# Kernel optimization log

Hardware: AMD Instinct MI355X
Metric: run time of the kernel (lower is better)

Reference implementation:

```python
import jax, jax.numpy as jnp
import numpy as np
import math

NEG = -1e9
NUM_SQUEEZE = 2


def seq_mask(lengths, max_len, dtype):
    return (jnp.arange(max_len)[None, :] < lengths[:, None]).astype(dtype)


def maximum_path(logp, attn_mask, x_lengths, y_lengths):
    """Monotonic alignment search (Viterbi DP). logp, attn_mask: [B, Tx, Ty]."""
    B, Tx, Ty = logp.shape
    logp = jnp.where(attn_mask > 0, logp, NEG)
    cols = jnp.moveaxis(logp, 2, 0)  # [Ty, B, Tx]

    v0 = jnp.where(jnp.arange(Tx)[None, :] == 0, 0.0, NEG).astype(logp.dtype)
    v0 = jnp.broadcast_to(v0, (B, Tx))

    def fwd(v, col):
        v_shift = jnp.concatenate([jnp.full((B, 1), NEG, logp.dtype), v[:, :-1]], axis=1)
        v_new = col + jnp.maximum(v, v_shift)
        return v_new, v_new

    _, values = jax.lax.scan(fwd, v0, cols)  # [Ty, B, Tx] DP table

    def bwd(index, j):
        active = j < y_lengths  # [B]
        row = jax.nn.one_hot(index, Tx, dtype=logp.dtype) * active[:, None].astype(logp.dtype)
        vprev = values[jnp.maximum(j - 1, 0)]  # [B, Tx]
        v_here = jnp.take_along_axis(vprev, index[:, None], axis=1)[:, 0]
        v_left = jnp.take_along_axis(vprev, jnp.maximum(index - 1, 0)[:, None], axis=1)[:, 0]
        dec = (index != 0) & ((index == j) | (v_here < v_left)) & active & (j > 0)
        return jnp.where(dec, index - 1, index), row

    js = jnp.arange(Ty - 1, -1, -1)
    _, rows = jax.lax.scan(bwd, x_lengths - 1, js)  # reversed j order
    path = jnp.moveaxis(jnp.flip(rows, 0), 0, 2)  # [B, Tx, Ty]
    return path * attn_mask


def setup_inputs() -> dict:
    key = jax.random.key(0)
    ks = jax.random.split(key, 6)
    B, C, Ten, Tde = 32, 80, 512, 2048
    return {
        "o_mean": jax.random.normal(ks[0], (B, C, Ten), jnp.float32),
        "o_log_scale": jax.random.normal(ks[1], (B, C, Ten), jnp.float32) * 0.1,
        "o_dur_log": jax.random.normal(ks[2], (B, 1, Ten), jnp.float32),
        "z": jax.random.normal(ks[3], (B, C, Tde), jnp.float32),
        "x_lengths": jax.random.randint(ks[4], (B,), Ten // 2, Ten + 1, jnp.int32),
        "y_lengths": jax.random.randint(ks[5], (B,), Tde // 2, Tde + 1, jnp.int32),
    }


def reference(o_mean, o_log_scale, o_dur_log, z, x_lengths, y_lengths):
    B, C, Ten = o_mean.shape
    Tde = z.shape[2]
    dt = o_mean.dtype

    # preprocess: floor y_lengths to multiple of num_squeeze
    y_lengths = (y_lengths // NUM_SQUEEZE) * NUM_SQUEEZE

    x_mask = seq_mask(x_lengths, Ten, dt)[:, None, :]   # [B,1,Tx]
    y_mask = seq_mask(y_lengths, Tde, dt)[:, None, :]   # [B,1,Ty]
    attn_mask = x_mask[:, 0, :, None] * y_mask[:, 0, None, :]  # [B,Tx,Ty]

    z = z * y_mask  # decoder output is masked

    # log-likelihood terms (torch.no_grad in original)
    o_scale = jnp.exp(-2.0 * o_log_scale)                       # [B,C,Tx]
    logp1 = jnp.sum(-0.5 * math.log(2 * math.pi) - o_log_scale, axis=1)[:, :, None]
    logp2 = jnp.einsum('bct,bcs->bts', o_scale, -0.5 * z * z)   # [B,Tx,Ty]
    logp3 = jnp.einsum('bct,bcs->bts', o_mean * o_scale, z)
    logp4 = jnp.sum(-0.5 * o_mean * o_mean * o_scale, axis=1)[:, :, None]
    logp = logp1 + logp2 + logp3 + logp4

    attn = maximum_path(logp, attn_mask, x_lengths, y_lengths)  # [B,Tx,Ty] hard path

    # compute_outputs
    y_mean = jnp.einsum('bts,bct->bcs', attn, o_mean)           # [B,C,Ty]
    y_log_scale = jnp.einsum('bts,bct->bcs', attn, o_log_scale)
    o_attn_dur = jnp.log1p(jnp.sum(attn, axis=-1))[:, None, :] * x_mask  # [B,1,Tx]

    return (
        jnp.transpose(z, (0, 2, 1)),            # z: [B,Ty,C]
        jnp.transpose(y_mean, (0, 2, 1)),       # y_mean: [B,Ty,C]
        jnp.transpose(y_log_scale, (0, 2, 1)),  # y_log_scale: [B,Ty,C]
        jnp.transpose(attn, (0, 2, 1)),         # alignments: [B,Ty,Tx]
        jnp.transpose(o_dur_log, (0, 2, 1)),    # durations_log: [B,Tx,1]
        jnp.transpose(o_attn_dur, (0, 2, 1)),   # total_durations_log: [B,Tx,1]
    )
```

## Files before the change

kernel.cpp:

```cpp
#include <hip/hip_runtime.h>
#include <math.h>

#define BB  32
#define CC  80
#define TXX 512
#define TYY 2048
#define NEGV -1e9f

typedef float v2f __attribute__((ext_vector_type(2)));

__global__ __launch_bounds__(256) void k_prep(
    const float* __restrict__ om, const float* __restrict__ ols,
    float* __restrict__ SA, float* __restrict__ SB,
    float* __restrict__ L1, float* __restrict__ L4,
    float* __restrict__ OMTf, float* __restrict__ OLSTf,
    int* __restrict__ DUR)
{
    int b = blockIdx.y;
    int t0 = blockIdx.x * 64;
    int tid = threadIdx.x;
    int cl = tid >> 6;
    int tl = tid & 63;
    __shared__ float sm[64][81], sl[64][81], ssa[64][81];
    #pragma unroll
    for (int cp = 0; cp < 20; ++cp) {
        int c = cp * 4 + cl;
        size_t gidx = ((size_t)b * CC + c) * TXX + t0 + tl;
        float m = om[gidx], ls = ols[gidx];
        float sa = expf(-2.0f * ls);
        SA[gidx] = sa;
        SB[gidx] = m * sa;
        sm[tl][c] = m; sl[tl][c] = ls; ssa[tl][c] = sa;
    }
    __syncthreads();
    if (tid < 64) {
        float l1 = 0.f, l4 = 0.f;
        #pragma unroll 4
        for (int c = 0; c < CC; ++c) {
            float m = sm[tid][c], ls = sl[tid][c], sa = ssa[tid][c];
            l1 += (-0.9189385332046727f - ls);
            l4 += ((-0.5f * m) * m) * sa;
        }
        int g = b * TXX + t0 + tid;
        L1[g] = l1; L4[g] = l4; DUR[g] = 0;
    }
    size_t obase = (size_t)b * TXX * CC + (size_t)t0 * CC;
    for (int e = tid; e < 64 * CC; e += 256) {
        int t = e / CC, c = e - t * CC;
        OMTf[obase + e]  = sm[t][c];
        OLSTf[obase + e] = sl[t][c];
    }
}

__global__ __launch_bounds__(256) void k_logp(
    const float* __restrict__ SA, const float* __restrict__ SB,
    const float* __restrict__ L1, const float* __restrict__ L4,
    const float* __restrict__ z,
    const int* __restrict__ xlp, const int* __restrict__ ylp,
    float* __restrict__ logp)
{
    int b = blockIdx.z;
    int ylen = (ylp[b] >> 1) << 1;
    int s0 = blockIdx.y * 128;
    if (s0 >= ylen) return;
    int t0 = blockIdx.x * 64;
    int xlen = xlp[b];
    int tid = threadIdx.x;

    __shared__ float sA[16][64], sB[16][64], sZ[16][128], sW[16][128];

    v2f acc2[4][4], acc3[4][4];
    #pragma unroll
    for (int i = 0; i < 4; ++i)
        #pragma unroll
        for (int p = 0; p < 4; ++p) { acc2[i][p] = (v2f){0.f, 0.f}; acc3[i][p] = (v2f){0.f, 0.f}; }

    int tt = (tid & 15) << 2;
    int ss = (tid >> 4) << 3;
    int r  = tid >> 4;
    int c4 = (tid & 15) << 2;
    int s8 = (tid & 15) << 3;

    for (int c0 = 0; c0 < CC; c0 += 16) {
        const float* pa = SA + ((size_t)b * CC + (c0 + r)) * TXX + t0 + c4;
        const float* pb = SB + ((size_t)b * CC + (c0 + r)) * TXX + t0 + c4;
        float4 va = *(const float4*)pa;
        float4 vb = *(const float4*)pb;
        *(float4*)&sA[r][c4] = va;
        *(float4*)&sB[r][c4] = vb;

        const float* pz = z + ((size_t)b * CC + (c0 + r)) * TYY + s0 + s8;
        float4 q0 = *(const float4*)pz;
        float4 q1 = *(const float4*)(pz + 4);
        float zf[8] = {q0.x, q0.y, q0.z, q0.w, q1.x, q1.y, q1.z, q1.w};
        #pragma unroll
        for (int i = 0; i < 8; ++i) {
            sZ[r][s8 + i] = zf[i];
            sW[r][s8 + i] = (-0.5f * zf[i]) * zf[i];
        }
        __syncthreads();
        #pragma unroll
        for (int kc = 0; kc < 16; ++kc) {
            float4 a2 = *(const float4*)&sA[kc][tt];
            float4 a3 = *(const float4*)&sB[kc][tt];
            const v2f* zp = (const v2f*)&sZ[kc][ss];
            const v2f* wp = (const v2f*)&sW[kc][ss];
            v2f bz[4] = {zp[0], zp[1], zp[2], zp[3]};
            v2f bw[4] = {wp[0], wp[1], wp[2], wp[3]};
            float av2[4] = {a2.x, a2.y, a2.z, a2.w};
            float av3[4] = {a3.x, a3.y, a3.z, a3.w};
            #pragma unroll
            for (int i = 0; i < 4; ++i) {
                v2f d2 = {av2[i], av2[i]};
                v2f d3 = {av3[i], av3[i]};
                #pragma unroll
                for (int p = 0; p < 4; ++p) {
                    acc2[i][p] = __builtin_elementwise_fma(d2, bw[p], acc2[i][p]);
                    acc3[i][p] = __builtin_elementwise_fma(d3, bz[p], acc3[i][p]);
                }
            }
        }
        __syncthreads();
    }

    float l1a[4], l4a[4]; int bad[4];
    #pragma unroll
    for (int i = 0; i < 4; ++i) {
        int t = t0 + tt + i;
        l1a[i] = L1[b * TXX + t];
        l4a[i] = L4[b * TXX + t];
        bad[i] = (t >= xlen);
    }
    #pragma unroll
    for (int p = 0; p < 4; ++p) {
        #pragma unroll
        for (int h = 0; h < 2; ++h) {
            int s = s0 + ss + 2 * p + h;
            float vals[4];
            #pragma unroll
            for (int i = 0; i < 4; ++i) {
                float a2v = h ? acc2[i][p].y : acc2[i][p].x;
                float a3v = h ? acc3[i][p].y : acc3[i][p].x;
                float v = ((l1a[i] + a2v) + a3v) + l4a[i];
                vals[i] = bad[i] ? NEGV : v;
            }
            float4 o; o.x = vals[0]; o.y = vals[1]; o.z = vals[2]; o.w = vals[3];
            *(float4*)&logp[((size_t)b * TYY + s) * TXX + t0 + tt] = o;
        }
    }
}

__device__ __forceinline__ unsigned dp_bits(const float v[8], float left) {
    unsigned by = (v[0] < left) ? 1u : 0u;
    by |= (v[1] < v[0]) ? 2u   : 0u;
    by |= (v[2] < v[1]) ? 4u   : 0u;
    by |= (v[3] < v[2]) ? 8u   : 0u;
    by |= (v[4] < v[3]) ? 16u  : 0u;
    by |= (v[5] < v[4]) ? 32u  : 0u;
    by |= (v[6] < v[5]) ? 64u  : 0u;
    by |= (v[7] < v[6]) ? 128u : 0u;
    return by;
}
__device__ __forceinline__ void dp_core(float v[8], float4 c0, float4 c1, float left) {
    float m0 = fmaxf(v[0], left);
    float m1 = fmaxf(v[1], v[0]);
    float m2 = fmaxf(v[2], v[1]);
    float m3 = fmaxf(v[3], v[2]);
    float m4 = fmaxf(v[4], v[3]);
    float m5 = fmaxf(v[5], v[4]);
    float m6 = fmaxf(v[6], v[5]);
    float m7 = fmaxf(v[7], v[6]);
    v[0] = c0.x + m0; v[1] = c0.y + m1; v[2] = c0.z + m2; v[3] = c0.w + m3;
    v[4] = c1.x + m4; v[5] = c1.y + m5; v[6] = c1.z + m6; v[7] = c1.w + m7;
}

__global__ __launch_bounds__(64) void k_fwd(
    const float* __restrict__ logp, const int* __restrict__ ylp,
    unsigned char* __restrict__ BITS)
{
    int b = blockIdx.x, lane = threadIdx.x;
    int n = (ylp[b] >> 1) << 1;
    int nm1 = n - 1;
    const float* lp = logp + (size_t)b * TYY * TXX + lane * 8;
    unsigned char* BITSb = BITS + (size_t)b * TYY * 64;
    __shared__ unsigned char lbits[128 * 64];

    float v[8];
    #pragma unroll
    for (int k = 0; k < 8; ++k) v[k] = NEGV;
    if (lane == 0) v[0] = 0.0f;

    float4 p0[16], p1[16];
    #pragma unroll
    for (int i = 0; i < 16; ++i) {
        int r0 = (i < nm1) ? i : nm1;
        p0[i] = *(const float4*)(lp + (size_t)r0 * TXX);
        p1[i] = *(const float4*)(lp + (size_t)r0 * TXX + 4);
    }

    int gs = 0;
    for (; gs + 64 <= n; gs += 64) {
        int hb = gs & 127;
        unsigned char* lb_first = lbits + lane + (((hb + 127) & 127) << 6);
        unsigned char* lb_rest  = lbits + lane + (hb << 6);
        #pragma unroll
        for (int j4 = 0; j4 < 4; ++j4) {
            #pragma unroll
            for (int uu = 0; uu < 16; ++uu) {
                const int j = j4 * 16 + uu;
                float4 c0 = p0[uu], c1 = p1[uu];
                int pr = gs + j + 16; if (pr > nm1) pr = nm1;
                p0[uu] = *(const float4*)(lp + (size_t)pr * TXX);
                p1[uu] = *(const float4*)(lp + (size_t)pr * TXX + 4);
                float left = __shfl_up(v[7], 1, 64);
                if (lane == 0) left = NEGV;
                if (j > 0 || gs > 0) {
                    unsigned by = dp_bits(v, left);
                    if (j == 0) *lb_first = (unsigned char)by;
                    else        lb_rest[(j - 1) << 6] = (unsigned char)by;
                }
                dp_core(v, c0, c1, left);
            }
        }
        if (gs >= 64) {
            int ps = hb ^ 64;
            const uint4* srcl = (const uint4*)(lbits + (size_t)((ps + lane) << 6));
            uint4 q0 = srcl[0], q1 = srcl[1], q2 = srcl[2], q3 = srcl[3];
            uint4* dstl = (uint4*)(BITSb + ((size_t)(gs - 64 + lane) << 6));
            dstl[0] = q0; dstl[1] = q1; dstl[2] = q2; dstl[3] = q3;
        }
    }
    {
        int pbase = gs - 64;
        int ps = pbase & 127;
        if (lane < 63) {
            const uint4* srcl = (const uint4*)(lbits + (size_t)((ps + lane) << 6));
            uint4 q0 = srcl[0], q1 = srcl[1], q2 = srcl[2], q3 = srcl[3];
            uint4* dstl = (uint4*)(BITSb + ((size_t)(pbase + lane) << 6));
            dstl[0] = q0; dstl[1] = q1; dstl[2] = q2; dstl[3] = q3;
        }
    }
    unsigned char* brow = BITSb + lane;
    #pragma unroll
    for (int j = 0; j < 64; ++j) {
        int scur = gs + j;
        if (scur >= n) break;
        const int uu = j & 15;
        float4 c0 = p0[uu], c1 = p1[uu];
        int pr = scur + 16; if (pr > nm1) pr = nm1;
        p0[uu] = *(const float4*)(lp + (size_t)pr * TXX);
        p1[uu] = *(const float4*)(lp + (size_t)pr * TXX + 4);
        float left = __shfl_up(v[7], 1, 64);
        if (lane == 0) left = NEGV;
        unsigned by = dp_bits(v, left);
        brow[(size_t)(scur - 1) << 6] = (unsigned char)by;
        dp_core(v, c0, c1, left);
    }
}

__global__ __launch_bounds__(64) void k_bwd(
    const unsigned char* __restrict__ BITS, const int* __restrict__ xlp,
    const int* __restrict__ ylp, int* __restrict__ TSTAR, int* __restrict__ DUR)
{
    int b = blockIdx.x, lane = threadIdx.x;
    int ylen = (ylp[b] >> 1) << 1;
    int xlen = xlp[b];
    const unsigned char* bb = BITS + (size_t)b * TYY * 64;
    int* tst = TSTAR + b * TYY;
    int idx = xlen - 1;
    int j0 = ylen - 1;
    while (j0 >= 0) {
        int steps = (j0 + 1 < 32) ? (j0 + 1) : 32;
        int row = j0 - 1 - lane;
        int bw = idx >> 5; if (bw > 0) --bw;
        int base_bit = bw << 5;
        unsigned w0 = 0u, w1 = 0u;
        if (lane < steps && row >= 0) {
            const unsigned* rp = (const unsigned*)(bb + (size_t)row * 64);
            w0 = rp[bw]; w1 = rp[bw + 1];
        }
        unsigned long long wq = (((unsigned long long)w1) << 32) | w0;
        int saved = 0;
        #pragma unroll
        for (int k = 0; k < 32; ++k) {
            if (k >= steps) break;
            int j = j0 - k;
            if (lane == k) saved = idx;
            unsigned long long wk = __shfl(wq, k, 64);
            unsigned bit = (unsigned)(wk >> (idx - base_bit)) & 1u;
            int dec = (idx != 0 && j > 0 && (idx == j || bit)) ? 1 : 0;
            idx -= dec;
        }
        if (lane < steps) {
            tst[j0 - lane] = saved;
            atomicAdd(&DUR[b * TXX + saved], 1);
        }
        j0 -= steps;
    }
}

__global__ __launch_bounds__(256) void k_small(
    const float* __restrict__ odur, const int* __restrict__ xlp,
    const int* __restrict__ DUR, float* __restrict__ out4,
    float* __restrict__ out5)
{
    int gid = blockIdx.x * 256 + threadIdx.x;
    int b = gid >> 9, t = gid & 511;
    out4[gid] = odur[gid];
    int xlen = xlp[b];
    float d = (float)DUR[gid];
    out5[gid] = (t < xlen) ? log1pf(d) : 0.0f;
}

__global__ __launch_bounds__(256) void k_out_sc(
    const float* __restrict__ z, const float* __restrict__ OMTf,
    const float* __restrict__ OLSTf, const int* __restrict__ TSTAR,
    const int* __restrict__ ylp,
    float* __restrict__ out0, float* __restrict__ out1,
    float* __restrict__ out2)
{
    int b = blockIdx.y;
    int s0 = blockIdx.x * 32;
    int tid = threadIdx.x;
    int ylen = (ylp[b] >> 1) << 1;
    __shared__ int sT[32];
    __shared__ float zt[32][81];
    if (tid < 32) {
        int s = s0 + tid;
        sT[tid] = (s < ylen) ? TSTAR[b * TYY + s] : 0;
    }
    int c_l = tid >> 5, s_l = tid & 31;
    #pragma unroll
    for (int cp = 0; cp < 10; ++cp) {
        int c = cp * 8 + c_l;
        zt[s_l][c] = z[((size_t)b * CC + c) * TYY + s0 + s_l];
    }
    __syncthreads();
    for (int e = tid; e < 32 * 80; e += 256) {
        int sl = e / 80;
        int cc = e - sl * 80;
        int s = s0 + sl;
        bool valid = s < ylen;
        int t = sT[sl];
        size_t o = ((size_t)b * TYY + s) * 80 + cc;
        size_t g = ((size_t)b * TXX + t) * 80 + cc;
        out0[o] = valid ? zt[sl][cc] : 0.0f;
        out1[o] = valid ? OMTf[g]    : 0.0f;
        out2[o] = valid ? OLSTf[g]   : 0.0f;
    }
}

__global__ __launch_bounds__(256) void k_attn(
    const int* __restrict__ TSTAR, const int* __restrict__ ylp,
    float* __restrict__ out3)
{
    int b = blockIdx.y;
    int s0 = blockIdx.x * 16;
    int tid = threadIdx.x;
    int ylen = (ylp[b] >> 1) << 1;
    #pragma unroll
    for (int r = 0; r < 16; ++r) {
        int s = s0 + r;
        int tr = (s < ylen) ? TSTAR[b * TYY + s] : -1;
        int t = tid << 1;
        float2 val;
        val.x = (t == tr) ? 1.0f : 0.0f;
        val.y = (t + 1 == tr) ? 1.0f : 0.0f;
        ((float2*)(out3 + ((size_t)b * TYY + s) * TXX))[tid] = val;
    }
}

extern "C" void kernel_launch(void* const* d_in, const int* in_sizes, int n_in,
                              void* d_out, int out_size, void* d_ws, size_t ws_size,
                              hipStream_t stream)
{
    const float* om   = (const float*)d_in[0];
    const float* ols  = (const float*)d_in[1];
    const float* odur = (const float*)d_in[2];
    const float* z    = (const float*)d_in[3];
    const int* xl = (const int*)d_in[4];
    const int* yl = (const int*)d_in[5];

    float* out0 = (float*)d_out;
    float* out1 = out0 + 5242880;
    float* out2 = out0 + 10485760;
    float* out3 = out0 + 15728640;
    float* out4 = out0 + 49283072;
    float* out5 = out0 + 49299456;

    float* SA   = out0;
    float* SB   = out0 + 1310720;
    float* logp = out3;

    char* ws = (char*)d_ws;
    float* L1 = (float*)ws;
    float* L4 = (float*)(ws + 65536);
    float* OMTf  = (float*)(ws + 131072);
    float* OLSTf = (float*)(ws + 5373952);
    unsigned char* BITS = (unsigned char*)(ws + 10616832);
    int* TSTAR = (int*)(ws + 14811136);
    int* DUR   = (int*)(ws + 15073280);

    hipLaunchKernelGGL(k_prep, dim3(8, 32), dim3(256), 0, stream,
                       om, ols, SA, SB, L1, L4, OMTf, OLSTf, DUR);
    hipLaunchKernelGGL(k_logp, dim3(8, 16, 32), dim3(256), 0, stream,
                       SA, SB, L1, L4, z, xl, yl, logp);
    hipLaunchKernelGGL(k_fwd, dim3(32), dim3(64), 0, stream, logp, yl, BITS);
    hipLaunchKernelGGL(k_bwd, dim3(32), dim3(64), 0, stream, BITS, xl, yl, TSTAR, DUR);
    hipLaunchKernelGGL(k_small, dim3(64), dim3(256), 0, stream, odur, xl, DUR, out4, out5);
    hipLaunchKernelGGL(k_out_sc, dim3(64, 32), dim3(256), 0, stream,
                       z, OMTf, OLSTf, TSTAR, yl, out0, out1, out2);
    hipLaunchKernelGGL(k_attn, dim3(128, 32), dim3(256), 0, stream, TSTAR, yl, out3);
}
```

Before: 808.2 us.

## Wavefront-pipeline Viterbi forward across 8 waves with ballot-packed decision bits

The forward DP now runs 512 threads per batch instead of 64. Each of the 8 waves owns 64 Tx columns with one element per lane, and the waves are skewed along Ty in 64-step blocks so they form a diagonal pipeline. Boundary values are handed between waves through shared memory, with a __syncthreads after each round. Decision bits are gathered with __ballot into 64-bit words laid out as [b][wave][Ty], and the backward kernel reads the new layout. This shortens each thread's serial chain of work, in exchange for 7 extra pipeline-fill rounds, a block-wide barrier per round and more per-step shuffles.

```diff
diff --git a/kernel.cpp b/kernel.cpp
--- a/kernel.cpp
+++ b/kernel.cpp
@@ -150,136 +150,88 @@
     }
 }
 
-__device__ __forceinline__ unsigned dp_bits(const float v[8], float left) {
-    unsigned by = (v[0] < left) ? 1u : 0u;
-    by |= (v[1] < v[0]) ? 2u   : 0u;
-    by |= (v[2] < v[1]) ? 4u   : 0u;
-    by |= (v[3] < v[2]) ? 8u   : 0u;
-    by |= (v[4] < v[3]) ? 16u  : 0u;
-    by |= (v[5] < v[4]) ? 32u  : 0u;
-    by |= (v[6] < v[5]) ? 64u  : 0u;
-    by |= (v[7] < v[6]) ? 128u : 0u;
-    return by;
-}
-__device__ __forceinline__ void dp_core(float v[8], float4 c0, float4 c1, float left) {
-    float m0 = fmaxf(v[0], left);
-    float m1 = fmaxf(v[1], v[0]);
-    float m2 = fmaxf(v[2], v[1]);
-    float m3 = fmaxf(v[3], v[2]);
-    float m4 = fmaxf(v[4], v[3]);
-    float m5 = fmaxf(v[5], v[4]);
-    float m6 = fmaxf(v[6], v[5]);
-    float m7 = fmaxf(v[7], v[6]);
-    v[0] = c0.x + m0; v[1] = c0.y + m1; v[2] = c0.z + m2; v[3] = c0.w + m3;
-    v[4] = c1.x + m4; v[5] = c1.y + m5; v[6] = c1.z + m6; v[7] = c1.w + m7;
-}
-
-__global__ __launch_bounds__(64) void k_fwd(
+__global__ __launch_bounds__(512) void k_fwd(
     const float* __restrict__ logp, const int* __restrict__ ylp,
-    unsigned char* __restrict__ BITS)
-{
-    int b = blockIdx.x, lane = threadIdx.x;
+    unsigned long long* __restrict__ BITS64)
+{
+    int b = blockIdx.x;
+    int tid = threadIdx.x;
+    int w = tid >> 6, lane = tid & 63;
     int n = (ylp[b] >> 1) << 1;
     int nm1 = n - 1;
-    const float* lp = logp + (size_t)b * TYY * TXX + lane * 8;
-    unsigned char* BITSb = BITS + (size_t)b * TYY * 64;
-    __shared__ unsigned char lbits[128 * 64];
-
-    float v[8];
-    #pragma unroll
-    for (int k = 0; k < 8; ++k) v[k] = NEGV;
-    if (lane == 0) v[0] = 0.0f;
-
-    float4 p0[16], p1[16];
-    #pragma unroll
-    for (int i = 0; i < 16; ++i) {
-        int r0 = (i < nm1) ? i : nm1;
-        p0[i] = *(const float4*)(lp + (size_t)r0 * TXX);
-        p1[i] = *(const float4*)(lp + (size_t)r0 * TXX + 4);
-    }
-
-    int gs = 0;
-    for (; gs + 64 <= n; gs += 64) {
-        int hb = gs & 127;
-        unsigned char* lb_first = lbits + lane + (((hb + 127) & 127) << 6);
-        unsigned char* lb_rest  = lbits + lane + (hb << 6);
-        #pragma unroll
-        for (int j4 = 0; j4 < 4; ++j4) {
+    int nb = (n + 63) >> 6;
+    const float* lpt = logp + (size_t)b * TYY * TXX + tid;
+    unsigned long long* bout = BITS64 + ((size_t)b * 8 + w) * TYY;
+
+    __shared__ float bound[8][256];
+    if (lane == 63) bound[w][255] = NEGV;
+    __syncthreads();
+
+    float v = (tid == 0) ? 0.0f : NEGV;
+    float c[16];
+    unsigned blo = 0u, bhi = 0u;
+    int rounds = nb + 7;
+    for (int r = 0; r < rounds; ++r) {
+        int blk = r - w;
+        if (blk >= 0 && blk < nb) {
+            int S0 = blk << 6;
+            if (blk == 0) {
+                #pragma unroll
+                for (int i = 0; i < 16; ++i) {
+                    int ps = (i < nm1) ? i : nm1;
+                    c[i] = lpt[(size_t)ps * TXX];
+                }
+            }
+            float BL = NEGV;
+            if (w > 0) BL = bound[w - 1][(S0 - 1 + lane) & 255];
             #pragma unroll
-            for (int uu = 0; uu < 16; ++uu) {
-                const int j = j4 * 16 + uu;
-                float4 c0 = p0[uu], c1 = p1[uu];
-                int pr = gs + j + 16; if (pr > nm1) pr = nm1;
-                p0[uu] = *(const float4*)(lp + (size_t)pr * TXX);
-                p1[uu] = *(const float4*)(lp + (size_t)pr * TXX + 4);
-                float left = __shfl_up(v[7], 1, 64);
-                if (lane == 0) left = NEGV;
-                if (j > 0 || gs > 0) {
-                    unsigned by = dp_bits(v, left);
-                    if (j == 0) *lb_first = (unsigned char)by;
-                    else        lb_rest[(j - 1) << 6] = (unsigned char)by;
+            for (int j = 0; j < 64; ++j) {
+                int s = S0 + j;
+                if (s < n) {
+                    float cc = c[j & 15];
+                    int ps = s + 16; if (ps > nm1) ps = nm1;
+                    c[j & 15] = lpt[(size_t)ps * TXX];
+                    float bl = __shfl(BL, j, 64);
+                    float left = __shfl_up(v, 1, 64);
+                    if (lane == 0) left = bl;
+                    unsigned long long m = __ballot(v < left);
+                    if (lane == j) { blo = (unsigned)m; bhi = (unsigned)(m >> 32); }
+                    v = cc + fmaxf(v, left);
+                    if (lane == 63) bound[w][s & 255] = v;
                 }
-                dp_core(v, c0, c1, left);
             }
-        }
-        if (gs >= 64) {
-            int ps = hb ^ 64;
-            const uint4* srcl = (const uint4*)(lbits + (size_t)((ps + lane) << 6));
-            uint4 q0 = srcl[0], q1 = srcl[1], q2 = srcl[2], q3 = srcl[3];
-            uint4* dstl = (uint4*)(BITSb + ((size_t)(gs - 64 + lane) << 6));
-            dstl[0] = q0; dstl[1] = q1; dstl[2] = q2; dstl[3] = q3;
-        }
-    }
-    {
-        int pbase = gs - 64;
-        int ps = pbase & 127;
-        if (lane < 63) {
-            const uint4* srcl = (const uint4*)(lbits + (size_t)((ps + lane) << 6));
-            uint4 q0 = srcl[0], q1 = srcl[1], q2 = srcl[2], q3 = srcl[3];
-            uint4* dstl = (uint4*)(BITSb + ((size_t)(pbase + lane) << 6));
-            dstl[0] = q0; dstl[1] = q1; dstl[2] = q2; dstl[3] = q3;
-        }
-    }
-    unsigned char* brow = BITSb + lane;
-    #pragma unroll
-    for (int j = 0; j < 64; ++j) {
-        int scur = gs + j;
-        if (scur >= n) break;
-        const int uu = j & 15;
-        float4 c0 = p0[uu], c1 = p1[uu];
-        int pr = scur + 16; if (pr > nm1) pr = nm1;
-        p0[uu] = *(const float4*)(lp + (size_t)pr * TXX);
-        p1[uu] = *(const float4*)(lp + (size_t)pr * TXX + 4);
-        float left = __shfl_up(v[7], 1, 64);
-        if (lane == 0) left = NEGV;
-        unsigned by = dp_bits(v, left);
-        brow[(size_t)(scur - 1) << 6] = (unsigned char)by;
-        dp_core(v, c0, c1, left);
+            int row = S0 - 1 + lane;
+            if (row >= 0 && S0 + lane < n)
+                bout[row] = (((unsigned long long)bhi) << 32) | blo;
+        }
+        __syncthreads();
     }
 }
 
 __global__ __launch_bounds__(64) void k_bwd(
-    const unsigned char* __restrict__ BITS, const int* __restrict__ xlp,
+    const unsigned long long* __restrict__ BITS64, const int* __restrict__ xlp,
     const int* __restrict__ ylp, int* __restrict__ TSTAR, int* __restrict__ DUR)
 {
     int b = blockIdx.x, lane = threadIdx.x;
     int ylen = (ylp[b] >> 1) << 1;
     int xlen = xlp[b];
-    const unsigned char* bb = BITS + (size_t)b * TYY * 64;
+    const unsigned long long* bb = BITS64 + (size_t)b * 8 * TYY;
     int* tst = TSTAR + b * TYY;
     int idx = xlen - 1;
     int j0 = ylen - 1;
     while (j0 >= 0) {
         int steps = (j0 + 1 < 32) ? (j0 + 1) : 32;
         int row = j0 - 1 - lane;
-        int bw = idx >> 5; if (bw > 0) --bw;
-        int base_bit = bw << 5;
-        unsigned w0 = 0u, w1 = 0u;
+        int bw5 = idx >> 5; if (bw5 > 0) --bw5;
+        int base_bit = bw5 << 5;
+        int c0 = base_bit >> 6;
+        int amt = base_bit & 63;
+        unsigned long long lo = 0ull, hi = 0ull;
         if (lane < steps && row >= 0) {
-            const unsigned* rp = (const unsigned*)(bb + (size_t)row * 64);
-            w0 = rp[bw]; w1 = rp[bw + 1];
-        }
-        unsigned long long wq = (((unsigned long long)w1) << 32) | w0;
+            lo = bb[(size_t)c0 * TYY + row];
+            if (amt) hi = bb[(size_t)(c0 + 1) * TYY + row];
+        }
+        unsigned long long wq = amt ? ((lo >> 32) | (hi << 32)) : lo;
         int saved = 0;
         #pragma unroll
         for (int k = 0; k < 32; ++k) {
@@ -397,7 +349,7 @@
     float* L4 = (float*)(ws + 65536);
     float* OMTf  = (float*)(ws + 131072);
     float* OLSTf = (float*)(ws + 5373952);
-    unsigned char* BITS = (unsigned char*)(ws + 10616832);
+    unsigned long long* BITS64 = (unsigned long long*)(ws + 10616832);
     int* TSTAR = (int*)(ws + 14811136);
     int* DUR   = (int*)(ws + 15073280);
 
@@ -405,8 +357,8 @@
                        om, ols, SA, SB, L1, L4, OMTf, OLSTf, DUR);
     hipLaunchKernelGGL(k_logp, dim3(8, 16, 32), dim3(256), 0, stream,
                        SA, SB, L1, L4, z, xl, yl, logp);
-    hipLaunchKernelGGL(k_fwd, dim3(32), dim3(64), 0, stream, logp, yl, BITS);
-    hipLaunchKernelGGL(k_bwd, dim3(32), dim3(64), 0, stream, BITS, xl, yl, TSTAR, DUR);
+    hipLaunchKernelGGL(k_fwd, dim3(32), dim3(512), 0, stream, logp, yl, BITS64);
+    hipLaunchKernelGGL(k_bwd, dim3(32), dim3(64), 0, stream, BITS64, xl, yl, TSTAR, DUR);
     hipLaunchKernelGGL(k_small, dim3(64), dim3(256), 0, stream, odur, xl, DUR, out4, out5);
     hipLaunchKernelGGL(k_out_sc, dim3(64, 32), dim3(256), 0, stream,
                        z, OMTf, OLSTf, TSTAR, yl, out0, out1, out2);
```

Result: slower. 1.267 ms (+56.8%).
